# Performance work log

Measured on AMD Instinct MI355X. Metric: run time of the kernel, lower is better.

Reference implementation:

```python
import jax, jax.numpy as jnp
import numpy as np

B, S, D, H = 4, 2048, 1024, 16
HD = D // H

def setup_inputs() -> dict:
    key = jax.random.key(0)
    ks = jax.random.split(key, 6)
    scale = 1.0 / np.sqrt(D)
    x = jax.random.normal(ks[0], (B, S, D), dtype=jnp.float32)
    q_w = jax.random.normal(ks[1], (D, D), dtype=jnp.float32) * scale
    k_w = jax.random.normal(ks[2], (D, D), dtype=jnp.float32) * scale
    v_w = jax.random.normal(ks[3], (D, D), dtype=jnp.float32) * scale
    o_w = jax.random.normal(ks[4], (D, D), dtype=jnp.float32) * scale
    zb = jnp.zeros((D,), dtype=jnp.float32)
    return {"x": x, "q_w": q_w, "q_b": zb, "k_w": k_w, "k_b": zb,
            "v_w": v_w, "v_b": zb, "o_w": o_w, "o_b": zb}

def reference(x, q_w, q_b, k_w, k_b, v_w, v_b, o_w, o_b):
    b, s, d = x.shape
    # projections; weights stored as (in, out) so y = x @ W + b
    q = (x @ q_w + q_b).reshape(b, s, H, HD).transpose(0, 2, 1, 3)  # [b,h,s,hd]
    k = (x @ k_w + k_b).reshape(b, s, H, HD).transpose(0, 2, 1, 3)
    v = (x @ v_w + v_b).reshape(b, s, H, HD).transpose(0, 2, 1, 3)
    attn = jnp.einsum('bhqd,bhkd->bhqk', q, k) * (HD ** -0.5)  # [b,h,s,s]
    attn = jax.nn.softmax(attn, axis=-1)
    out = jnp.einsum('bhqk,bhkd->bhqd', attn, v)  # [b,h,s,hd]
    out = out.transpose(0, 2, 1, 3).reshape(b, s, d)
    return out @ o_w + o_b
```

## Files before the change

kernel.cpp:

```cpp
#include <hip/hip_runtime.h>
#include <hip/hip_bf16.h>

typedef __bf16 bf16;
typedef __bf16 bf16x4 __attribute__((ext_vector_type(4)));
typedef __bf16 bf16x8 __attribute__((ext_vector_type(8)));
typedef float f32x4 __attribute__((ext_vector_type(4)));

#define NB 4
#define SEQ 2048
#define DM 1024
#define NH 16
#define HDIM 64
#define MTOT (NB*SEQ)

#define QSCALE 0.18033688011112042f

#define ASYNC16(ldsp, gp) __builtin_amdgcn_global_load_lds( \
    (const __attribute__((address_space(1))) void*)(gp),    \
    (__attribute__((address_space(3))) void*)(ldsp), 16, 0, 0)

__global__ void cvt_x_kernel(const float* __restrict__ x, bf16* __restrict__ xb, int n4) {
  int i = blockIdx.x * blockDim.x + threadIdx.x;
  int stride = gridDim.x * blockDim.x;
  for (; i < n4; i += stride) {
    float4 v = ((const float4*)x)[i];
    bf16x4 o = {(bf16)v.x, (bf16)v.y, (bf16)v.z, (bf16)v.w};
    ((bf16x4*)xb)[i] = o;
  }
}

__global__ void cvt_w_kernel(const float* __restrict__ w0, const float* __restrict__ w1,
                             const float* __restrict__ w2, const float* __restrict__ w3,
                             bf16* __restrict__ wt) {
  __shared__ float t[32][33];
  const float* w = blockIdx.z == 0 ? w0 : blockIdx.z == 1 ? w1 : blockIdx.z == 2 ? w2 : w3;
  bf16* o = wt + (size_t)blockIdx.z * DM * DM;
  int n0 = blockIdx.x * 32, k0 = blockIdx.y * 32;
  int tx = threadIdx.x, ty = threadIdx.y;
  #pragma unroll
  for (int i = 0; i < 4; i++) t[ty + 8*i][tx] = w[(size_t)(k0 + ty + 8*i) * DM + n0 + tx];
  __syncthreads();
  #pragma unroll
  for (int i = 0; i < 4; i++) o[(size_t)(n0 + ty + 8*i) * DM + k0 + tx] = (bf16)t[tx][ty + 8*i];
}

template<int EPI>
__global__ __launch_bounds__(256) void gemm128(
    const bf16* __restrict__ A, const bf16* __restrict__ Bt,
    const float* __restrict__ bq, const float* __restrict__ bk, const float* __restrict__ bv,
    bf16* __restrict__ oq, bf16* __restrict__ ok, bf16* __restrict__ ovt,
    float* __restrict__ of) {
  const int tid = threadIdx.x;
  const int lane = tid & 63;
  const int wid = tid >> 6;
  const int wr = wid >> 1, wc = wid & 1;
  const int bm = blockIdx.y * 128;
  const int bn = blockIdx.x * 128;

  __shared__ __align__(16) bf16 As[2][128 * 32];
  __shared__ __align__(16) bf16 Bs[2][128 * 32];

  f32x4 acc[4][4] = {};

  const bf16* ga = A  + (size_t)(bm + (tid >> 2)) * DM + (tid & 3) * 8;
  const bf16* gb = Bt + (size_t)(bn + (tid >> 2)) * DM + (tid & 3) * 8;

  ASYNC16(&As[0][tid * 8], ga);
  ASYNC16(&As[0][2048 + tid * 8], ga + 64 * DM);
  ASYNC16(&Bs[0][tid * 8], gb);
  ASYNC16(&Bs[0][2048 + tid * 8], gb + 64 * DM);

  const int r0 = lane & 15;
  const int kc = (lane >> 4) * 8;

  for (int kt = 0; kt < DM / 32; ++kt) {
    const int cur = kt & 1;
    __syncthreads();
    if (kt + 1 < DM / 32) {
      const int nk = (kt + 1) * 32;
      ASYNC16(&As[cur ^ 1][tid * 8], ga + nk);
      ASYNC16(&As[cur ^ 1][2048 + tid * 8], ga + 64 * DM + nk);
      ASYNC16(&Bs[cur ^ 1][tid * 8], gb + nk);
      ASYNC16(&Bs[cur ^ 1][2048 + tid * 8], gb + 64 * DM + nk);
    }
    bf16x8 af[4], bfr[4];
    #pragma unroll
    for (int i = 0; i < 4; i++) {
      af[i]  = *(const bf16x8*)&As[cur][(wr * 64 + i * 16 + r0) * 32 + kc];
      bfr[i] = *(const bf16x8*)&Bs[cur][(wc * 64 + i * 16 + r0) * 32 + kc];
    }
    #pragma unroll
    for (int i = 0; i < 4; i++)
      #pragma unroll
      for (int j = 0; j < 4; j++)
        acc[i][j] = __builtin_amdgcn_mfma_f32_16x16x32_bf16(af[i], bfr[j], acc[i][j], 0, 0, 0);
  }

  if (EPI == 0) {
    const int which = bn >> 10;
    const float* bp = which == 0 ? bq : which == 1 ? bk : bv;
    const float scale = (which == 0) ? QSCALE : 1.0f;
    #pragma unroll
    for (int j = 0; j < 4; j++) {
      const int n = bn + wc * 64 + j * 16 + r0;
      const int dcol = n & 1023;
      const int h = dcol >> 6, hd = dcol & 63;
      const float bias = bp[dcol];
      const int qk_d = ((hd >> 5) * 4 + ((hd >> 3) & 3)) * 128 + (hd & 7);
      const int v_d  = (hd >> 4) * 1024 + (hd & 15) * 8;
      #pragma unroll
      for (int i = 0; i < 4; i++)
        #pragma unroll
        for (int r = 0; r < 4; r++) {
          const int m = bm + wr * 64 + i * 16 + (lane >> 4) * 4 + r;
          const int b_ = m >> 11, s_ = m & 2047;
          const float v = (acc[i][j][r] + bias) * scale;
          if (which <= 1) {
            const size_t off = ((size_t)(b_ * NH + h) * (SEQ / 16) + (s_ >> 4)) * 1024
                             + qk_d + (s_ & 15) * 8;
            (which == 0 ? oq : ok)[off] = (bf16)v;
          } else {
            const size_t off = ((size_t)(b_ * NH + h) * (SEQ / 64) + (s_ >> 6)) * 4096
                             + v_d + ((s_ >> 5) & 1) * 512 + ((s_ >> 3) & 3) * 128 + (s_ & 7);
            ovt[off] = (bf16)v;
          }
        }
    }
  } else {
    #pragma unroll
    for (int j = 0; j < 4; j++) {
      const int n = bn + wc * 64 + j * 16 + r0;
      const float bias = bq[n];
      #pragma unroll
      for (int i = 0; i < 4; i++)
        #pragma unroll
        for (int r = 0; r < 4; r++) {
          const int m = bm + wr * 64 + i * 16 + (lane >> 4) * 4 + r;
          of[(size_t)m * DM + n] = acc[i][j][r] + bias;
        }
    }
  }
}

__global__ __launch_bounds__(256) void attn_kernel(
    const bf16* __restrict__ Q, const bf16* __restrict__ Kf, const bf16* __restrict__ Vf,
    bf16* __restrict__ O) {
  const int tid = threadIdx.x;
  const int lane = tid & 63;
  const int wid = tid >> 6;
  const int g = lane >> 4;
  const int q = lane & 15;
  const int qt = blockIdx.x;
  const int h = blockIdx.y;
  const int b = blockIdx.z;

  const bf16* qp = Q  + ((size_t)(b * NH + h) * (SEQ / 16) + qt * 4) * 1024;
  const bf16* kp = Kf + (size_t)(b * NH + h) * (SEQ / 16) * 1024;
  const bf16* vp = Vf + (size_t)(b * NH + h) * (SEQ / 64) * 4096;

  __shared__ __align__(16) bf16 Ks[2][4096];
  __shared__ __align__(16) bf16 Vs[2][4096];
  __shared__ __align__(16) bf16 Pp[4][16 * 72];

  ASYNC16(&Ks[1][tid * 8], qp + tid * 8);
  ASYNC16(&Ks[1][2048 + tid * 8], qp + 2048 + tid * 8);
  ASYNC16(&Ks[0][tid * 8], kp + tid * 8);
  ASYNC16(&Ks[0][2048 + tid * 8], kp + 2048 + tid * 8);
  ASYNC16(&Vs[0][tid * 8], vp + tid * 8);
  ASYNC16(&Vs[0][2048 + tid * 8], vp + 2048 + tid * 8);
  __syncthreads();

  const bf16x8 aq0 = *(const bf16x8*)&Ks[1][wid * 1024 + 0 * 512 + g * 128 + q * 8];
  const bf16x8 aq1 = *(const bf16x8*)&Ks[1][wid * 1024 + 1 * 512 + g * 128 + q * 8];
  __syncthreads();

  float m_run = -1e30f, l_run = 0.f;
  f32x4 oacc[4] = {};

  bf16* pw = &Pp[wid][q * 72 + g * 4];
  const bf16* prd = &Pp[wid][q * 72 + g * 8];

  for (int kt = 0; kt < SEQ / 64; ++kt) {
    const int cur = kt & 1;
    if (kt + 1 < SEQ / 64) {
      const bf16* gk = kp + (size_t)(kt + 1) * 4096;
      ASYNC16(&Ks[cur ^ 1][tid * 8], gk + tid * 8);
      ASYNC16(&Ks[cur ^ 1][2048 + tid * 8], gk + 2048 + tid * 8);
      const bf16* gv = vp + (size_t)(kt + 1) * 4096;
      ASYNC16(&Vs[cur ^ 1][tid * 8], gv + tid * 8);
      ASYNC16(&Vs[cur ^ 1][2048 + tid * 8], gv + 2048 + tid * 8);
    }

    f32x4 sc[4] = {};
    __builtin_amdgcn_s_setprio(1);
    #pragma unroll
    for (int nf = 0; nf < 4; nf++) {
      const bf16x8 bk0 = *(const bf16x8*)&Ks[cur][nf * 1024 + 0 * 512 + g * 128 + q * 8];
      sc[nf] = __builtin_amdgcn_mfma_f32_16x16x32_bf16(bk0, aq0, sc[nf], 0, 0, 0);
      const bf16x8 bk1 = *(const bf16x8*)&Ks[cur][nf * 1024 + 1 * 512 + g * 128 + q * 8];
      sc[nf] = __builtin_amdgcn_mfma_f32_16x16x32_bf16(bk1, aq1, sc[nf], 0, 0, 0);
    }
    __builtin_amdgcn_s_setprio(0);

    float pmax = fmaxf(fmaxf(sc[0][0], sc[0][1]), fmaxf(sc[0][2], sc[0][3]));
    #pragma unroll
    for (int nf = 1; nf < 4; nf++)
      pmax = fmaxf(pmax, fmaxf(fmaxf(sc[nf][0], sc[nf][1]), fmaxf(sc[nf][2], sc[nf][3])));
    pmax = fmaxf(pmax, __shfl_xor(pmax, 16));
    pmax = fmaxf(pmax, __shfl_xor(pmax, 32));

    if (__any(pmax > m_run + 8.f)) {
      const float mnew = fmaxf(m_run, pmax);
      const float fac = exp2f(m_run - mnew);
      l_run *= fac;
      #pragma unroll
      for (int df = 0; df < 4; df++)
        #pragma unroll
        for (int r = 0; r < 4; r++)
          oacc[df][r] *= fac;
      m_run = mnew;
    }

    float psum = 0.f;
    #pragma unroll
    for (int nf = 0; nf < 4; nf++) {
      bf16x4 pk;
      #pragma unroll
      for (int r = 0; r < 4; r++) {
        const float pv = exp2f(sc[nf][r] - m_run);
        psum += pv;
        pk[r] = (bf16)pv;
      }
      *(bf16x4*)(pw + nf * 16) = pk;
    }
    psum += __shfl_xor(psum, 16);
    psum += __shfl_xor(psum, 32);
    l_run += psum;

    __builtin_amdgcn_s_setprio(1);
    #pragma unroll
    for (int c = 0; c < 2; c++) {
      const bf16x8 pf = *(const bf16x8*)(prd + c * 32);
      #pragma unroll
      for (int df = 0; df < 4; df++) {
        const bf16x8 bv = *(const bf16x8*)&Vs[cur][df * 1024 + c * 512 + g * 128 + q * 8];
        oacc[df] = __builtin_amdgcn_mfma_f32_16x16x32_bf16(bv, pf, oacc[df], 0, 0, 0);
      }
    }
    __builtin_amdgcn_s_setprio(0);
    __syncthreads();
  }

  const float inv = 1.0f / l_run;
  const int qrow = qt * 64 + wid * 16 + q;
  bf16* ob = (bf16*)&O[((size_t)b * SEQ + qrow) * DM + h * HDIM + g * 4];
  #pragma unroll
  for (int df = 0; df < 4; df++) {
    bf16x4 ov;
    #pragma unroll
    for (int r = 0; r < 4; r++) ov[r] = (bf16)(oacc[df][r] * inv);
    *(bf16x4*)(ob + df * 16) = ov;
  }
}

extern "C" void kernel_launch(void* const* d_in, const int* in_sizes, int n_in,
                              void* d_out, int out_size, void* d_ws, size_t ws_size,
                              hipStream_t stream) {
  (void)in_sizes; (void)n_in; (void)out_size; (void)ws_size;
  const float* x   = (const float*)d_in[0];
  const float* q_w = (const float*)d_in[1];
  const float* q_b = (const float*)d_in[2];
  const float* k_w = (const float*)d_in[3];
  const float* k_b = (const float*)d_in[4];
  const float* v_w = (const float*)d_in[5];
  const float* v_b = (const float*)d_in[6];
  const float* o_w = (const float*)d_in[7];
  const float* o_b = (const float*)d_in[8];
  float* out = (float*)d_out;

  char* p = (char*)d_ws;
  bf16* xb = (bf16*)p;  p += (size_t)MTOT * DM * 2;
  bf16* wt = (bf16*)p;  p += (size_t)4 * DM * DM * 2;
  bf16* qq = (bf16*)p;  p += (size_t)MTOT * DM * 2;
  bf16* kk = (bf16*)p;  p += (size_t)MTOT * DM * 2;
  bf16* vt = (bf16*)p;  p += (size_t)MTOT * DM * 2;

  cvt_x_kernel<<<1024, 256, 0, stream>>>(x, xb, MTOT * DM / 4);
  cvt_w_kernel<<<dim3(32, 32, 4), dim3(32, 8), 0, stream>>>(q_w, k_w, v_w, o_w, wt);

  gemm128<0><<<dim3(24, 64), 256, 0, stream>>>(xb, wt, q_b, k_b, v_b, qq, kk, vt, nullptr);

  attn_kernel<<<dim3(SEQ / 64, NH, NB), 256, 0, stream>>>(qq, kk, vt, xb);

  gemm128<1><<<dim3(8, 64), 256, 0, stream>>>(xb, wt + (size_t)3 * DM * DM, o_b, nullptr, nullptr,
                                              nullptr, nullptr, nullptr, out);
}
```

Measured before the change: 372.8 us.

## Switch attention to 32x32x16 MFMA with 128-row query tiles per block

Rewrites the attention kernel to use 32x32x16 bf16 MFMA instead of 16x16x32, with each wave owning 32 query rows, so a block covers 128 queries. The Q/K/V layouts written by the QKV GEMM epilogue change to match the new fragment shapes. This halves K/V tile reloads per query and cuts per-row softmax reduction shuffles. In exchange it uses more accumulator registers and launches half as many blocks, which may lower occupancy and parallelism.

```diff
diff --git a/kernel.cpp b/kernel.cpp
--- a/kernel.cpp
+++ b/kernel.cpp
@@ -5,6 +5,7 @@
 typedef __bf16 bf16x4 __attribute__((ext_vector_type(4)));
 typedef __bf16 bf16x8 __attribute__((ext_vector_type(8)));
 typedef float f32x4 __attribute__((ext_vector_type(4)));
+typedef float f32x16 __attribute__((ext_vector_type(16)));
 
 #define NB 4
 #define SEQ 2048
@@ -12,6 +13,7 @@
 #define NH 16
 #define HDIM 64
 #define MTOT (NB*SEQ)
+#define BH_STRIDE (SEQ * HDIM)
 
 #define QSCALE 0.18033688011112042f
 
@@ -106,8 +108,8 @@
       const int dcol = n & 1023;
       const int h = dcol >> 6, hd = dcol & 63;
       const float bias = bp[dcol];
-      const int qk_d = ((hd >> 5) * 4 + ((hd >> 3) & 3)) * 128 + (hd & 7);
-      const int v_d  = (hd >> 4) * 1024 + (hd & 15) * 8;
+      const int qk_d = (hd >> 4) * 512 + ((hd >> 3) & 1) * 256 + (hd & 7);
+      const int v_d  = (hd >> 5) * 2048 + (hd & 31) * 8;
       #pragma unroll
       for (int i = 0; i < 4; i++)
         #pragma unroll
@@ -116,12 +118,13 @@
           const int b_ = m >> 11, s_ = m & 2047;
           const float v = (acc[i][j][r] + bias) * scale;
           if (which <= 1) {
-            const size_t off = ((size_t)(b_ * NH + h) * (SEQ / 16) + (s_ >> 4)) * 1024
-                             + qk_d + (s_ & 15) * 8;
+            const size_t off = (size_t)(b_ * NH + h) * BH_STRIDE
+                             + (s_ >> 5) * 2048 + (s_ & 31) * 8 + qk_d;
             (which == 0 ? oq : ok)[off] = (bf16)v;
           } else {
-            const size_t off = ((size_t)(b_ * NH + h) * (SEQ / 64) + (s_ >> 6)) * 4096
-                             + v_d + ((s_ >> 5) & 1) * 512 + ((s_ >> 3) & 3) * 128 + (s_ & 7);
+            const size_t off = (size_t)(b_ * NH + h) * BH_STRIDE
+                             + (s_ >> 6) * 4096 + ((s_ >> 4) & 3) * 512
+                             + ((s_ >> 3) & 1) * 256 + (s_ & 7) + v_d;
             ovt[off] = (bf16)v;
           }
         }
@@ -148,65 +151,71 @@
   const int tid = threadIdx.x;
   const int lane = tid & 63;
   const int wid = tid >> 6;
-  const int g = lane >> 4;
-  const int q = lane & 15;
+  const int hi = lane >> 5;
+  const int q5 = lane & 31;
   const int qt = blockIdx.x;
   const int h = blockIdx.y;
   const int b = blockIdx.z;
 
-  const bf16* qp = Q  + ((size_t)(b * NH + h) * (SEQ / 16) + qt * 4) * 1024;
-  const bf16* kp = Kf + (size_t)(b * NH + h) * (SEQ / 16) * 1024;
-  const bf16* vp = Vf + (size_t)(b * NH + h) * (SEQ / 64) * 4096;
-
-  __shared__ __align__(16) bf16 Ks[2][4096];
-  __shared__ __align__(16) bf16 Vs[2][4096];
-  __shared__ __align__(16) bf16 Pp[4][16 * 72];
-
-  ASYNC16(&Ks[1][tid * 8], qp + tid * 8);
-  ASYNC16(&Ks[1][2048 + tid * 8], qp + 2048 + tid * 8);
-  ASYNC16(&Ks[0][tid * 8], kp + tid * 8);
-  ASYNC16(&Ks[0][2048 + tid * 8], kp + 2048 + tid * 8);
-  ASYNC16(&Vs[0][tid * 8], vp + tid * 8);
-  ASYNC16(&Vs[0][2048 + tid * 8], vp + 2048 + tid * 8);
+  const bf16* qp = Q  + (size_t)(b * NH + h) * BH_STRIDE + qt * 8192;
+  const bf16* kp = Kf + (size_t)(b * NH + h) * BH_STRIDE;
+  const bf16* vp = Vf + (size_t)(b * NH + h) * BH_STRIDE;
+
+  __shared__ __align__(16) bf16 KsF[8192];
+  __shared__ __align__(16) bf16 VsF[8192];
+  __shared__ __align__(16) bf16 Pp[4][32 * 68];
+
+  ASYNC16(&KsF[tid * 8], qp + tid * 8);
+  ASYNC16(&KsF[2048 + tid * 8], qp + 2048 + tid * 8);
+  ASYNC16(&KsF[4096 + tid * 8], qp + 4096 + tid * 8);
+  ASYNC16(&KsF[6144 + tid * 8], qp + 6144 + tid * 8);
   __syncthreads();
-
-  const bf16x8 aq0 = *(const bf16x8*)&Ks[1][wid * 1024 + 0 * 512 + g * 128 + q * 8];
-  const bf16x8 aq1 = *(const bf16x8*)&Ks[1][wid * 1024 + 1 * 512 + g * 128 + q * 8];
+  bf16x8 qf[4];
+  #pragma unroll
+  for (int ks = 0; ks < 4; ks++)
+    qf[ks] = *(const bf16x8*)&KsF[wid * 2048 + ks * 512 + hi * 256 + q5 * 8];
   __syncthreads();
 
+  ASYNC16(&KsF[tid * 8], kp + tid * 8);
+  ASYNC16(&KsF[2048 + tid * 8], kp + 2048 + tid * 8);
+  ASYNC16(&VsF[tid * 8], vp + tid * 8);
+  ASYNC16(&VsF[2048 + tid * 8], vp + 2048 + tid * 8);
+  __syncthreads();
+
   float m_run = -1e30f, l_run = 0.f;
-  f32x4 oacc[4] = {};
-
-  bf16* pw = &Pp[wid][q * 72 + g * 4];
-  const bf16* prd = &Pp[wid][q * 72 + g * 8];
+  f32x16 oaccA = {}, oaccB = {};
+
+  bf16* pwb = &Pp[wid][q5 * 68 + hi * 4];
+  const bf16* prd = &Pp[wid][q5 * 68 + hi * 8];
 
   for (int kt = 0; kt < SEQ / 64; ++kt) {
-    const int cur = kt & 1;
+    const int curo = (kt & 1) * 4096;
     if (kt + 1 < SEQ / 64) {
+      const int nxo = curo ^ 4096;
       const bf16* gk = kp + (size_t)(kt + 1) * 4096;
-      ASYNC16(&Ks[cur ^ 1][tid * 8], gk + tid * 8);
-      ASYNC16(&Ks[cur ^ 1][2048 + tid * 8], gk + 2048 + tid * 8);
+      ASYNC16(&KsF[nxo + tid * 8], gk + tid * 8);
+      ASYNC16(&KsF[nxo + 2048 + tid * 8], gk + 2048 + tid * 8);
       const bf16* gv = vp + (size_t)(kt + 1) * 4096;
-      ASYNC16(&Vs[cur ^ 1][tid * 8], gv + tid * 8);
-      ASYNC16(&Vs[cur ^ 1][2048 + tid * 8], gv + 2048 + tid * 8);
-    }
-
-    f32x4 sc[4] = {};
+      ASYNC16(&VsF[nxo + tid * 8], gv + tid * 8);
+      ASYNC16(&VsF[nxo + 2048 + tid * 8], gv + 2048 + tid * 8);
+    }
+
+    f32x16 sc0 = {}, sc1 = {};
     __builtin_amdgcn_s_setprio(1);
     #pragma unroll
-    for (int nf = 0; nf < 4; nf++) {
-      const bf16x8 bk0 = *(const bf16x8*)&Ks[cur][nf * 1024 + 0 * 512 + g * 128 + q * 8];
-      sc[nf] = __builtin_amdgcn_mfma_f32_16x16x32_bf16(bk0, aq0, sc[nf], 0, 0, 0);
-      const bf16x8 bk1 = *(const bf16x8*)&Ks[cur][nf * 1024 + 1 * 512 + g * 128 + q * 8];
-      sc[nf] = __builtin_amdgcn_mfma_f32_16x16x32_bf16(bk1, aq1, sc[nf], 0, 0, 0);
+    for (int ks = 0; ks < 4; ks++) {
+      const bf16x8 kf0 = *(const bf16x8*)&KsF[curo + ks * 512 + hi * 256 + q5 * 8];
+      sc0 = __builtin_amdgcn_mfma_f32_32x32x16_bf16(kf0, qf[ks], sc0, 0, 0, 0);
+      const bf16x8 kf1 = *(const bf16x8*)&KsF[curo + 2048 + ks * 512 + hi * 256 + q5 * 8];
+      sc1 = __builtin_amdgcn_mfma_f32_32x32x16_bf16(kf1, qf[ks], sc1, 0, 0, 0);
     }
     __builtin_amdgcn_s_setprio(0);
 
-    float pmax = fmaxf(fmaxf(sc[0][0], sc[0][1]), fmaxf(sc[0][2], sc[0][3]));
-    #pragma unroll
-    for (int nf = 1; nf < 4; nf++)
-      pmax = fmaxf(pmax, fmaxf(fmaxf(sc[nf][0], sc[nf][1]), fmaxf(sc[nf][2], sc[nf][3])));
-    pmax = fmaxf(pmax, __shfl_xor(pmax, 16));
+    float pmax = sc0[0];
+    #pragma unroll
+    for (int r = 1; r < 16; r++) pmax = fmaxf(pmax, sc0[r]);
+    #pragma unroll
+    for (int r = 0; r < 16; r++) pmax = fmaxf(pmax, sc1[r]);
     pmax = fmaxf(pmax, __shfl_xor(pmax, 32));
 
     if (__any(pmax > m_run + 8.f)) {
@@ -214,52 +223,55 @@
       const float fac = exp2f(m_run - mnew);
       l_run *= fac;
       #pragma unroll
-      for (int df = 0; df < 4; df++)
-        #pragma unroll
-        for (int r = 0; r < 4; r++)
-          oacc[df][r] *= fac;
+      for (int r = 0; r < 16; r++) { oaccA[r] *= fac; oaccB[r] *= fac; }
       m_run = mnew;
     }
 
     float psum = 0.f;
     #pragma unroll
-    for (int nf = 0; nf < 4; nf++) {
-      bf16x4 pk;
-      #pragma unroll
-      for (int r = 0; r < 4; r++) {
-        const float pv = exp2f(sc[nf][r] - m_run);
-        psum += pv;
-        pk[r] = (bf16)pv;
+    for (int rg = 0; rg < 4; rg++) {
+      bf16x4 pk0, pk1;
+      #pragma unroll
+      for (int e = 0; e < 4; e++) {
+        const float pv0 = exp2f(sc0[rg * 4 + e] - m_run);
+        psum += pv0;
+        pk0[e] = (bf16)pv0;
+        const float pv1 = exp2f(sc1[rg * 4 + e] - m_run);
+        psum += pv1;
+        pk1[e] = (bf16)pv1;
       }
-      *(bf16x4*)(pw + nf * 16) = pk;
-    }
-    psum += __shfl_xor(psum, 16);
+      *(bf16x4*)(pwb + rg * 8) = pk0;
+      *(bf16x4*)(pwb + 32 + rg * 8) = pk1;
+    }
     psum += __shfl_xor(psum, 32);
     l_run += psum;
 
     __builtin_amdgcn_s_setprio(1);
     #pragma unroll
-    for (int c = 0; c < 2; c++) {
-      const bf16x8 pf = *(const bf16x8*)(prd + c * 32);
-      #pragma unroll
-      for (int df = 0; df < 4; df++) {
-        const bf16x8 bv = *(const bf16x8*)&Vs[cur][df * 1024 + c * 512 + g * 128 + q * 8];
-        oacc[df] = __builtin_amdgcn_mfma_f32_16x16x32_bf16(bv, pf, oacc[df], 0, 0, 0);
-      }
+    for (int kvs = 0; kvs < 4; kvs++) {
+      const bf16x8 pf = *(const bf16x8*)(prd + kvs * 16);
+      const bf16x8 vf0 = *(const bf16x8*)&VsF[curo + kvs * 512 + hi * 256 + q5 * 8];
+      oaccA = __builtin_amdgcn_mfma_f32_32x32x16_bf16(vf0, pf, oaccA, 0, 0, 0);
+      const bf16x8 vf1 = *(const bf16x8*)&VsF[curo + 2048 + kvs * 512 + hi * 256 + q5 * 8];
+      oaccB = __builtin_amdgcn_mfma_f32_32x32x16_bf16(vf1, pf, oaccB, 0, 0, 0);
     }
     __builtin_amdgcn_s_setprio(0);
     __syncthreads();
   }
 
   const float inv = 1.0f / l_run;
-  const int qrow = qt * 64 + wid * 16 + q;
-  bf16* ob = (bf16*)&O[((size_t)b * SEQ + qrow) * DM + h * HDIM + g * 4];
+  const int qrow = qt * 128 + wid * 32 + q5;
+  bf16* ob = (bf16*)&O[((size_t)b * SEQ + qrow) * DM + h * HDIM + hi * 4];
   #pragma unroll
-  for (int df = 0; df < 4; df++) {
-    bf16x4 ov;
-    #pragma unroll
-    for (int r = 0; r < 4; r++) ov[r] = (bf16)(oacc[df][r] * inv);
-    *(bf16x4*)(ob + df * 16) = ov;
+  for (int rg = 0; rg < 4; rg++) {
+    bf16x4 ovA, ovB;
+    #pragma unroll
+    for (int e = 0; e < 4; e++) {
+      ovA[e] = (bf16)(oaccA[rg * 4 + e] * inv);
+      ovB[e] = (bf16)(oaccB[rg * 4 + e] * inv);
+    }
+    *(bf16x4*)(ob + rg * 8) = ovA;
+    *(bf16x4*)(ob + 32 + rg * 8) = ovB;
   }
 }
 
@@ -290,7 +302,7 @@
 
   gemm128<0><<<dim3(24, 64), 256, 0, stream>>>(xb, wt, q_b, k_b, v_b, qq, kk, vt, nullptr);
 
-  attn_kernel<<<dim3(SEQ / 64, NH, NB), 256, 0, stream>>>(qq, kk, vt, xb);
+  attn_kernel<<<dim3(SEQ / 128, NH, NB), 256, 0, stream>>>(qq, kk, vt, xb);
 
   gemm128<1><<<dim3(8, 64), 256, 0, stream>>>(xb, wt + (size_t)3 * DM * DM, o_b, nullptr, nullptr,
                                               nullptr, nullptr, nullptr, out);
```

Result: no change. 379.5 us (+1.8%).
